# Performance work log

Measured on AMD Instinct MI355X. Metric: run time of the kernel, lower is better.

Reference implementation:

```python
import jax, jax.numpy as jnp
import numpy as np

N = 4_194_304
NUM_ITER = 6
DAMPING = 0.95
TOL = 1e-06
EPS = 1e-12


def _translate_x(dx):
    """4x4 homogeneous translation along the optical (x) axis."""
    return jnp.eye(4, dtype=dx.dtype).at[0, 3].set(dx)


def setup_inputs() -> dict:
    key = jax.random.key(0)
    k1, k2, k3 = jax.random.split(key, 3)
    # Ray origins: near x = -10, transverse spread within/around the aperture
    px = -10.0 + 0.5 * jax.random.normal(k1, (N, 1), dtype=jnp.float32)
    pyz = 8.0 * jax.random.normal(k2, (N, 2), dtype=jnp.float32)
    P = jnp.concatenate([px, pyz], axis=-1)
    # Ray directions: mostly +x, small transverse components, normalized
    vyz = 0.05 * jax.random.normal(k3, (N, 2), dtype=jnp.float32)
    V = jnp.concatenate([jnp.ones((N, 1), jnp.float32), vyz], axis=-1)
    V = V / jnp.linalg.norm(V, axis=-1, keepdims=True)
    tf = jnp.eye(4, dtype=jnp.float32)
    return {
        "P": P,
        "V": V,
        "tf": tf,
        "diameter": jnp.float32(50.0),
        "C": jnp.float32(0.02),
        "anchors": jnp.zeros((2,), jnp.float32),
        "scale": jnp.float32(1.0),
        "normalize": jnp.asarray(False),
    }


def reference(P, V, tf, diameter, C, anchors, scale, normalize):
    # normalize: curvature interpreted relative to semi-diameter
    C_eff = jnp.where(normalize, C * 2.0 / diameter, C)
    s2 = scale * scale

    def sag(r2):  # scaled spherical sag: f = scale * g(r2/scale^2)
        u = r2 / s2
        root = jnp.sqrt(jnp.clip(1.0 - C_eff * C_eff * u, EPS))
        return scale * C_eff * u / (1.0 + root)

    def sag_grad(y, z):  # (df/dy, df/dz) = C*(y,z) / (scale*sqrt(1-C^2 u))
        u = (y * y + z * z) / s2
        root = jnp.sqrt(jnp.clip(1.0 - C_eff * C_eff * u, EPS))
        k = C_eff / (scale * root)
        return k * y, k * z

    # anchors shift the surface along x by fractions of the edge sag (extent)
    extent = sag(jnp.square(diameter * 0.5))
    surface_tf = tf @ _translate_x(-anchors[0] * extent)
    next_tf = tf @ _translate_x((anchors[1] - anchors[0]) * extent)

    # Rays into surface-local frame
    R = surface_tf[:3, :3]
    tv = surface_tf[:3, 3]
    Pl = (P - tv) @ R  # [N,3] = R^T (P - t)
    Vl = V @ R
    vx, vy, vz = Vl[:, 0], Vl[:, 1], Vl[:, 2]

    safe_vx = jnp.where(jnp.abs(vx) > EPS, vx, EPS)
    t = -Pl[:, 0] / safe_vx  # init: intersection with plane x=0

    # Damped Newton on F(t) = sag(y(t),z(t)) - x(t)
    for _ in range(NUM_ITER):
        p = Pl + t[:, None] * Vl
        y, z = p[:, 1], p[:, 2]
        F = sag(y * y + z * z) - p[:, 0]
        gy, gz = sag_grad(y, z)
        dF = gy * vy + gz * vz - vx
        dF = jnp.where(jnp.abs(dF) > EPS, dF, EPS)
        t = t - DAMPING * F / dF

    p = Pl + t[:, None] * Vl
    y, z = p[:, 1], p[:, 2]
    r2 = y * y + z * z
    F = sag(r2) - p[:, 0]
    gy, gz = sag_grad(y, z)
    # implicit-surface normal: grad(sag(y,z) - x) = (-1, gy, gz), normalized
    n_local = jnp.stack([-jnp.ones_like(gy), gy, gz], axis=-1)
    n_local = n_local / jnp.linalg.norm(n_local, axis=-1, keepdims=True)
    normals = n_local @ R.T  # back to global frame

    valid = (r2 <= jnp.square(diameter * 0.5)) & (jnp.abs(F) < 100.0 * TOL)
    return t, normals, valid, surface_tf, next_tf
```

## Files before the change

### kernel.cpp

```cpp
#include <hip/hip_runtime.h>

#define F_EPS 1e-12f
#define F_DAMPING 0.95f
#define N_ITER 6
#define TPB 256

__launch_bounds__(TPB)
__global__ void trace_kernel(const float* __restrict__ P,
                             const float* __restrict__ V,
                             const float* __restrict__ tf,
                             const float* __restrict__ diameter,
                             const float* __restrict__ Cc,
                             const float* __restrict__ anchors,
                             const float* __restrict__ scale_p,
                             const unsigned char* __restrict__ normalize,
                             float* __restrict__ out,
                             int n)
{
    __shared__ float4 sbuf[TPB * 3];
    const int tid  = threadIdx.x;
    const int base = (blockIdx.x * TPB + tid) * 4;

    float R0,R1,R2,R3,R4,R5,R6,R7,R8, tv0,tv1,tv2;
    float C_eff, scale, half_d2, inv_s2;
    {
#pragma clang fp contract(off)
        float d  = diameter[0];
        float c  = Cc[0];
        float sc = scale_p[0];
        bool  nrm = (normalize[0] != 0);
        C_eff = nrm ? (c * 2.0f / d) : c;
        float s2 = sc * sc;
        float hr = d * 0.5f;
        half_d2 = hr * hr;
        float u = half_d2 / s2;
        float root = sqrtf(fmaxf(1.0f - (C_eff * C_eff) * u, F_EPS));
        float extent = sc * C_eff * u / (1.0f + root);
        float a0 = anchors[0], a1 = anchors[1];
        float dx0 = -a0 * extent;
        float dx1 = (a1 - a0) * extent;
        R0 = tf[0]; R1 = tf[1]; R2 = tf[2];
        R3 = tf[4]; R4 = tf[5]; R5 = tf[6];
        R6 = tf[8]; R7 = tf[9]; R8 = tf[10];
        tv0 = tf[0] * dx0 + tf[3];
        tv1 = tf[4] * dx0 + tf[7];
        tv2 = tf[8] * dx0 + tf[11];
        scale  = sc;
        inv_s2 = 1.0f / s2;
        if (blockIdx.x == 0 && tid < 16) {
            int i = tid >> 2, j = tid & 3;
            float v  = tf[tid];
            float sv = (j == 3) ? (tf[i * 4] * dx0 + v) : v;
            float nv = (j == 3) ? (tf[i * 4] * dx1 + v) : v;
            float* out_tail = out + (size_t)n * 5;
            out_tail[tid]      = sv;
            out_tail[16 + tid] = nv;
        }
    }
    float ce2   = C_eff * C_eff;
    float sC    = scale * C_eff;
    float a_num = sC * inv_s2;
    float ce2s  = ce2 * inv_s2;
    float Cs    = C_eff / scale;

    const bool full_block = ((blockIdx.x + 1) * (TPB * 4) <= n);

    float Px[4], Py[4], Pz[4], Vx[4], Vy[4], Vz[4];
    if (full_block) {
        const size_t bf4 = (size_t)blockIdx.x * (TPB * 3);
        const float4* P4 = reinterpret_cast<const float4*>(P);
        const float4* V4 = reinterpret_cast<const float4*>(V);
        float4 p0 = P4[bf4 + tid], p1 = P4[bf4 + TPB + tid], p2 = P4[bf4 + 2*TPB + tid];
        float4 q0 = V4[bf4 + tid], q1 = V4[bf4 + TPB + tid], q2 = V4[bf4 + 2*TPB + tid];
        sbuf[tid] = p0; sbuf[TPB + tid] = p1; sbuf[2*TPB + tid] = p2;
        __syncthreads();
        float4 a = sbuf[3*tid], b = sbuf[3*tid + 1], c = sbuf[3*tid + 2];
        __syncthreads();
        Px[0]=a.x; Py[0]=a.y; Pz[0]=a.z; Px[1]=a.w; Py[1]=b.x; Pz[1]=b.y;
        Px[2]=b.z; Py[2]=b.w; Pz[2]=c.x; Px[3]=c.y; Py[3]=c.z; Pz[3]=c.w;
        sbuf[tid] = q0; sbuf[TPB + tid] = q1; sbuf[2*TPB + tid] = q2;
        __syncthreads();
        a = sbuf[3*tid]; b = sbuf[3*tid + 1]; c = sbuf[3*tid + 2];
        __syncthreads();
        Vx[0]=a.x; Vy[0]=a.y; Vz[0]=a.z; Vx[1]=a.w; Vy[1]=b.x; Vz[1]=b.y;
        Vx[2]=b.z; Vy[2]=b.w; Vz[2]=c.x; Vx[3]=c.y; Vy[3]=c.z; Vz[3]=c.w;
    } else {
        for (int r = 0; r < 4; ++r) {
            int i = base + r;
            if (i < n) {
                Px[r] = P[(size_t)i*3 + 0]; Py[r] = P[(size_t)i*3 + 1]; Pz[r] = P[(size_t)i*3 + 2];
                Vx[r] = V[(size_t)i*3 + 0]; Vy[r] = V[(size_t)i*3 + 1]; Vz[r] = V[(size_t)i*3 + 2];
            } else {
                Px[r] = 0.0f; Py[r] = 0.0f; Pz[r] = 0.0f;
                Vx[r] = 1.0f; Vy[r] = 0.0f; Vz[r] = 0.0f;
            }
        }
    }

    float Plx[4], Ply[4], Plz[4], vx[4], vy[4], vz[4], tN[4];
#pragma unroll
    for (int r = 0; r < 4; ++r) {
        float px0 = Px[r] - tv0, py0 = Py[r] - tv1, pz0 = Pz[r] - tv2;
        Plx[r] = px0 * R0 + py0 * R3 + pz0 * R6;
        Ply[r] = px0 * R1 + py0 * R4 + pz0 * R7;
        Plz[r] = px0 * R2 + py0 * R5 + pz0 * R8;
        vx[r] = Vx[r] * R0 + Vy[r] * R3 + Vz[r] * R6;
        vy[r] = Vx[r] * R1 + Vy[r] * R4 + Vz[r] * R7;
        vz[r] = Vx[r] * R2 + Vy[r] * R5 + Vz[r] * R8;
        float safe_vx = (fabsf(vx[r]) > F_EPS) ? vx[r] : F_EPS;
        tN[r] = (-Plx[r]) * __builtin_amdgcn_rcpf(safe_vx);
    }

#pragma unroll
    for (int it = 0; it < N_ITER; ++it) {
#pragma unroll
        for (int r = 0; r < 4; ++r) {
            float pxx = fmaf(tN[r], vx[r], Plx[r]);
            float py  = fmaf(tN[r], vy[r], Ply[r]);
            float pz  = fmaf(tN[r], vz[r], Plz[r]);
            float r2  = fmaf(py, py, pz * pz);
            float m   = fmaxf(fmaf(-ce2s, r2, 1.0f), F_EPS);
            float rsq = __builtin_amdgcn_rsqf(m);
            float root = m * rsq;
            float k    = Cs * rsq;
            float ird  = __builtin_amdgcn_rcpf(1.0f + root);
            float F    = fmaf(a_num * r2, ird, -pxx);
            float dF = fmaf(k * py, vy[r], fmaf(k * pz, vz[r], -vx[r]));
            dF = (fabsf(dF) > F_EPS) ? dF : F_EPS;
            tN[r] = fmaf(-F_DAMPING * F, __builtin_amdgcn_rcpf(dF), tN[r]);
        }
    }

    float tres[4], nxo[4], nyo[4], nzo[4], val[4];
#pragma unroll
    for (int r = 0; r < 4; ++r) {
        float pxx = fmaf(tN[r], vx[r], Plx[r]);
        float py  = fmaf(tN[r], vy[r], Ply[r]);
        float pz  = fmaf(tN[r], vz[r], Plz[r]);
        float r2  = fmaf(py, py, pz * pz);
        float m   = fmaxf(fmaf(-ce2s, r2, 1.0f), F_EPS);
        float rsq = __builtin_amdgcn_rsqf(m);
        float root = m * rsq;
        float k    = Cs * rsq;
        float ird  = __builtin_amdgcn_rcpf(1.0f + root);
        float F    = fmaf(a_num * r2, ird, -pxx);
        float gy = k * py, gz = k * pz;
        float nn2 = fmaf(gy, gy, fmaf(gz, gz, 1.0f));
        float irn = __builtin_amdgcn_rsqf(nn2);
        float nlx = -irn, nly = gy * irn, nlz = gz * irn;
        nxo[r] = nlx * R0 + nly * R1 + nlz * R2;
        nyo[r] = nlx * R3 + nly * R4 + nlz * R5;
        nzo[r] = nlx * R6 + nly * R7 + nlz * R8;
        tres[r] = tN[r];
        val[r]  = ((r2 <= half_d2) && (fabsf(F) < 1e-4f)) ? 1.0f : 0.0f;
    }

    float* t_out = out;
    float* n_out = out + (size_t)n;
    float* v_out = out + (size_t)n * 4;
    if (full_block) {
        sbuf[3*tid]     = make_float4(nxo[0], nyo[0], nzo[0], nxo[1]);
        sbuf[3*tid + 1] = make_float4(nyo[1], nzo[1], nxo[2], nyo[2]);
        sbuf[3*tid + 2] = make_float4(nzo[2], nxo[3], nyo[3], nzo[3]);
        __syncthreads();
        const size_t bf4 = (size_t)blockIdx.x * (TPB * 3);
        float4* N4 = reinterpret_cast<float4*>(n_out);
        N4[bf4 + tid]         = sbuf[tid];
        N4[bf4 + TPB + tid]   = sbuf[TPB + tid];
        N4[bf4 + 2*TPB + tid] = sbuf[2*TPB + tid];
        *reinterpret_cast<float4*>(t_out + base) = make_float4(tres[0], tres[1], tres[2], tres[3]);
        *reinterpret_cast<float4*>(v_out + base) = make_float4(val[0], val[1], val[2], val[3]);
    } else {
        for (int r = 0; r < 4; ++r) {
            int i = base + r;
            if (i < n) {
                t_out[i] = tres[r];
                n_out[(size_t)i*3 + 0] = nxo[r];
                n_out[(size_t)i*3 + 1] = nyo[r];
                n_out[(size_t)i*3 + 2] = nzo[r];
                v_out[i] = val[r];
            }
        }
    }
}

extern "C" void kernel_launch(void* const* d_in, const int* in_sizes, int n_in,
                              void* d_out, int out_size, void* d_ws, size_t ws_size,
                              hipStream_t stream) {
    const float* P  = (const float*)d_in[0];
    const float* V  = (const float*)d_in[1];
    const float* tf = (const float*)d_in[2];
    const float* diameter = (const float*)d_in[3];
    const float* C  = (const float*)d_in[4];
    const float* anchors = (const float*)d_in[5];
    const float* scale = (const float*)d_in[6];
    const unsigned char* normalize = (const unsigned char*)d_in[7];
    int n = in_sizes[0] / 3;
    float* out = (float*)d_out;

    int rays_per_block = TPB * 4;
    int blocks = (n + rays_per_block - 1) / rays_per_block;
    trace_kernel<<<blocks, TPB, 0, stream>>>(P, V, tf, diameter, C, anchors, scale,
                                             normalize, out, n);
}
```

Measured before the change: 177.1 us.

## Process four tiles per block with register prefetch, drop LDS transpose

Each block now handles four tiles of rays and prefetches the next tile's P/V into registers while computing the current one, giving a software-pipelined loop. The shared-memory transpose and its barriers are removed: each thread loads its own three contiguous float4s directly and writes normals the same way. This cuts the grid size by four and hides load latency behind compute. The cost is higher register pressure and per-thread strided float4 accesses that coalesce less well than the old LDS-staged pattern.

```diff
diff --git a/kernel.cpp b/kernel.cpp
--- a/kernel.cpp
+++ b/kernel.cpp
@@ -4,6 +4,7 @@
 #define F_DAMPING 0.95f
 #define N_ITER 6
 #define TPB 256
+#define TILES 4
 
 __launch_bounds__(TPB)
 __global__ void trace_kernel(const float* __restrict__ P,
@@ -17,9 +18,7 @@
                              float* __restrict__ out,
                              int n)
 {
-    __shared__ float4 sbuf[TPB * 3];
-    const int tid  = threadIdx.x;
-    const int base = (blockIdx.x * TPB + tid) * 4;
+    const int tid = threadIdx.x;
 
     float R0,R1,R2,R3,R4,R5,R6,R7,R8, tv0,tv1,tv2;
     float C_eff, scale, half_d2, inv_s2;
@@ -57,130 +56,167 @@
             out_tail[16 + tid] = nv;
         }
     }
-    float ce2   = C_eff * C_eff;
-    float sC    = scale * C_eff;
-    float a_num = sC * inv_s2;
-    float ce2s  = ce2 * inv_s2;
-    float Cs    = C_eff / scale;
-
-    const bool full_block = ((blockIdx.x + 1) * (TPB * 4) <= n);
-
-    float Px[4], Py[4], Pz[4], Vx[4], Vy[4], Vz[4];
-    if (full_block) {
-        const size_t bf4 = (size_t)blockIdx.x * (TPB * 3);
-        const float4* P4 = reinterpret_cast<const float4*>(P);
-        const float4* V4 = reinterpret_cast<const float4*>(V);
-        float4 p0 = P4[bf4 + tid], p1 = P4[bf4 + TPB + tid], p2 = P4[bf4 + 2*TPB + tid];
-        float4 q0 = V4[bf4 + tid], q1 = V4[bf4 + TPB + tid], q2 = V4[bf4 + 2*TPB + tid];
-        sbuf[tid] = p0; sbuf[TPB + tid] = p1; sbuf[2*TPB + tid] = p2;
-        __syncthreads();
-        float4 a = sbuf[3*tid], b = sbuf[3*tid + 1], c = sbuf[3*tid + 2];
-        __syncthreads();
-        Px[0]=a.x; Py[0]=a.y; Pz[0]=a.z; Px[1]=a.w; Py[1]=b.x; Pz[1]=b.y;
-        Px[2]=b.z; Py[2]=b.w; Pz[2]=c.x; Px[3]=c.y; Py[3]=c.z; Pz[3]=c.w;
-        sbuf[tid] = q0; sbuf[TPB + tid] = q1; sbuf[2*TPB + tid] = q2;
-        __syncthreads();
-        a = sbuf[3*tid]; b = sbuf[3*tid + 1]; c = sbuf[3*tid + 2];
-        __syncthreads();
-        Vx[0]=a.x; Vy[0]=a.y; Vz[0]=a.z; Vx[1]=a.w; Vy[1]=b.x; Vz[1]=b.y;
-        Vx[2]=b.z; Vy[2]=b.w; Vz[2]=c.x; Vx[3]=c.y; Vy[3]=c.z; Vz[3]=c.w;
-    } else {
-        for (int r = 0; r < 4; ++r) {
-            int i = base + r;
-            if (i < n) {
-                Px[r] = P[(size_t)i*3 + 0]; Py[r] = P[(size_t)i*3 + 1]; Pz[r] = P[(size_t)i*3 + 2];
-                Vx[r] = V[(size_t)i*3 + 0]; Vy[r] = V[(size_t)i*3 + 1]; Vz[r] = V[(size_t)i*3 + 2];
-            } else {
-                Px[r] = 0.0f; Py[r] = 0.0f; Pz[r] = 0.0f;
-                Vx[r] = 1.0f; Vy[r] = 0.0f; Vz[r] = 0.0f;
-            }
-        }
-    }
-
-    float Plx[4], Ply[4], Plz[4], vx[4], vy[4], vz[4], tN[4];
-#pragma unroll
-    for (int r = 0; r < 4; ++r) {
-        float px0 = Px[r] - tv0, py0 = Py[r] - tv1, pz0 = Pz[r] - tv2;
-        Plx[r] = px0 * R0 + py0 * R3 + pz0 * R6;
-        Ply[r] = px0 * R1 + py0 * R4 + pz0 * R7;
-        Plz[r] = px0 * R2 + py0 * R5 + pz0 * R8;
-        vx[r] = Vx[r] * R0 + Vy[r] * R3 + Vz[r] * R6;
-        vy[r] = Vx[r] * R1 + Vy[r] * R4 + Vz[r] * R7;
-        vz[r] = Vx[r] * R2 + Vy[r] * R5 + Vz[r] * R8;
-        float safe_vx = (fabsf(vx[r]) > F_EPS) ? vx[r] : F_EPS;
-        tN[r] = (-Plx[r]) * __builtin_amdgcn_rcpf(safe_vx);
-    }
-
-#pragma unroll
-    for (int it = 0; it < N_ITER; ++it) {
-#pragma unroll
-        for (int r = 0; r < 4; ++r) {
-            float pxx = fmaf(tN[r], vx[r], Plx[r]);
-            float py  = fmaf(tN[r], vy[r], Ply[r]);
-            float pz  = fmaf(tN[r], vz[r], Plz[r]);
-            float r2  = fmaf(py, py, pz * pz);
-            float m   = fmaxf(fmaf(-ce2s, r2, 1.0f), F_EPS);
-            float rsq = __builtin_amdgcn_rsqf(m);
-            float root = m * rsq;
-            float k    = Cs * rsq;
-            float ird  = __builtin_amdgcn_rcpf(1.0f + root);
-            float F    = fmaf(a_num * r2, ird, -pxx);
-            float dF = fmaf(k * py, vy[r], fmaf(k * pz, vz[r], -vx[r]));
-            dF = (fabsf(dF) > F_EPS) ? dF : F_EPS;
-            tN[r] = fmaf(-F_DAMPING * F, __builtin_amdgcn_rcpf(dF), tN[r]);
-        }
-    }
-
-    float tres[4], nxo[4], nyo[4], nzo[4], val[4];
-#pragma unroll
-    for (int r = 0; r < 4; ++r) {
-        float pxx = fmaf(tN[r], vx[r], Plx[r]);
-        float py  = fmaf(tN[r], vy[r], Ply[r]);
-        float pz  = fmaf(tN[r], vz[r], Plz[r]);
-        float r2  = fmaf(py, py, pz * pz);
-        float m   = fmaxf(fmaf(-ce2s, r2, 1.0f), F_EPS);
-        float rsq = __builtin_amdgcn_rsqf(m);
-        float root = m * rsq;
-        float k    = Cs * rsq;
-        float ird  = __builtin_amdgcn_rcpf(1.0f + root);
-        float F    = fmaf(a_num * r2, ird, -pxx);
-        float gy = k * py, gz = k * pz;
-        float nn2 = fmaf(gy, gy, fmaf(gz, gz, 1.0f));
-        float irn = __builtin_amdgcn_rsqf(nn2);
-        float nlx = -irn, nly = gy * irn, nlz = gz * irn;
-        nxo[r] = nlx * R0 + nly * R1 + nlz * R2;
-        nyo[r] = nlx * R3 + nly * R4 + nlz * R5;
-        nzo[r] = nlx * R6 + nly * R7 + nlz * R8;
-        tres[r] = tN[r];
-        val[r]  = ((r2 <= half_d2) && (fabsf(F) < 1e-4f)) ? 1.0f : 0.0f;
-    }
-
+    const float ce2   = C_eff * C_eff;
+    const float sC    = scale * C_eff;
+    const float a_num = sC * inv_s2;
+    const float ce2s  = ce2 * inv_s2;
+    const float Cs    = C_eff / scale;
+
+    const float4* P4 = reinterpret_cast<const float4*>(P);
+    const float4* V4 = reinterpret_cast<const float4*>(V);
     float* t_out = out;
     float* n_out = out + (size_t)n;
     float* v_out = out + (size_t)n * 4;
-    if (full_block) {
-        sbuf[3*tid]     = make_float4(nxo[0], nyo[0], nzo[0], nxo[1]);
-        sbuf[3*tid + 1] = make_float4(nyo[1], nzo[1], nxo[2], nyo[2]);
-        sbuf[3*tid + 2] = make_float4(nzo[2], nxo[3], nyo[3], nzo[3]);
-        __syncthreads();
-        const size_t bf4 = (size_t)blockIdx.x * (TPB * 3);
-        float4* N4 = reinterpret_cast<float4*>(n_out);
-        N4[bf4 + tid]         = sbuf[tid];
-        N4[bf4 + TPB + tid]   = sbuf[TPB + tid];
-        N4[bf4 + 2*TPB + tid] = sbuf[2*TPB + tid];
-        *reinterpret_cast<float4*>(t_out + base) = make_float4(tres[0], tres[1], tres[2], tres[3]);
-        *reinterpret_cast<float4*>(v_out + base) = make_float4(val[0], val[1], val[2], val[3]);
-    } else {
-        for (int r = 0; r < 4; ++r) {
-            int i = base + r;
-            if (i < n) {
-                t_out[i] = tres[r];
-                n_out[(size_t)i*3 + 0] = nxo[r];
-                n_out[(size_t)i*3 + 1] = nyo[r];
-                n_out[(size_t)i*3 + 2] = nzo[r];
-                v_out[i] = val[r];
-            }
-        }
+
+
+    float4 c0,c1,c2,c3,c4,c5;
+    float4 x0,x1,x2,x3,x4,x5;
+
+    {
+        size_t u = ((size_t)blockIdx.x * TILES + 0) * TPB + tid;
+        long base = (long)u * 4;
+        if (base + 4 <= n) {
+            c0 = P4[u*3+0]; c1 = P4[u*3+1]; c2 = P4[u*3+2];
+            c3 = V4[u*3+0]; c4 = V4[u*3+1]; c5 = V4[u*3+2];
+        } else {
+            float tmp[12];
+            for (int r = 0; r < 4; ++r) {
+                long i = base + r;
+                if (i < n) {
+                    tmp[r*3+0] = P[i*3+0]; tmp[r*3+1] = P[i*3+1]; tmp[r*3+2] = P[i*3+2];
+                } else { tmp[r*3+0] = 0.0f; tmp[r*3+1] = 0.0f; tmp[r*3+2] = 0.0f; }
+            }
+            c0 = make_float4(tmp[0],tmp[1],tmp[2],tmp[3]);
+            c1 = make_float4(tmp[4],tmp[5],tmp[6],tmp[7]);
+            c2 = make_float4(tmp[8],tmp[9],tmp[10],tmp[11]);
+            for (int r = 0; r < 4; ++r) {
+                long i = base + r;
+                if (i < n) {
+                    tmp[r*3+0] = V[i*3+0]; tmp[r*3+1] = V[i*3+1]; tmp[r*3+2] = V[i*3+2];
+                } else { tmp[r*3+0] = 1.0f; tmp[r*3+1] = 0.0f; tmp[r*3+2] = 0.0f; }
+            }
+            c3 = make_float4(tmp[0],tmp[1],tmp[2],tmp[3]);
+            c4 = make_float4(tmp[4],tmp[5],tmp[6],tmp[7]);
+            c5 = make_float4(tmp[8],tmp[9],tmp[10],tmp[11]);
+        }
+    }
+
+#pragma unroll
+    for (int j = 0; j < TILES; ++j) {
+        if (j + 1 < TILES) {
+            size_t u1 = ((size_t)blockIdx.x * TILES + (j+1)) * TPB + tid;
+            long base1 = (long)u1 * 4;
+            if (base1 + 4 <= n) {
+                x0 = P4[u1*3+0]; x1 = P4[u1*3+1]; x2 = P4[u1*3+2];
+                x3 = V4[u1*3+0]; x4 = V4[u1*3+1]; x5 = V4[u1*3+2];
+            } else {
+                x0 = make_float4(0,0,0,0); x1 = x0; x2 = x0;
+                x3 = make_float4(1,0,0,1); x4 = make_float4(0,0,1,0); x5 = make_float4(0,0,1,0);
+                for (int r = 0; r < 4; ++r) {
+                    long i = base1 + r;
+                    if (i < n) {
+                        float px = P[i*3+0], py = P[i*3+1], pz = P[i*3+2];
+                        float qx = V[i*3+0], qy = V[i*3+1], qz = V[i*3+2];
+                        if (r==0) { x0.x=px; x0.y=py; x0.z=pz; x3.x=qx; x3.y=qy; x3.z=qz; }
+                        if (r==1) { x0.w=px; x1.x=py; x1.y=pz; x3.w=qx; x4.x=qy; x4.y=qz; }
+                        if (r==2) { x1.z=px; x1.w=py; x2.x=pz; x4.z=qx; x4.w=qy; x5.x=qz; }
+                        if (r==3) { x2.y=px; x2.z=py; x2.w=pz; x5.y=qx; x5.z=qy; x5.w=qz; }
+                    }
+                }
+            }
+        }
+
+        size_t u = ((size_t)blockIdx.x * TILES + j) * TPB + tid;
+        long base = (long)u * 4;
+        if (base < n) {
+            float Px[4], Py[4], Pz[4], Vx[4], Vy[4], Vz[4];
+            Px[0]=c0.x; Py[0]=c0.y; Pz[0]=c0.z; Px[1]=c0.w; Py[1]=c1.x; Pz[1]=c1.y;
+            Px[2]=c1.z; Py[2]=c1.w; Pz[2]=c2.x; Px[3]=c2.y; Py[3]=c2.z; Pz[3]=c2.w;
+            Vx[0]=c3.x; Vy[0]=c3.y; Vz[0]=c3.z; Vx[1]=c3.w; Vy[1]=c4.x; Vz[1]=c4.y;
+            Vx[2]=c4.z; Vy[2]=c4.w; Vz[2]=c5.x; Vx[3]=c5.y; Vy[3]=c5.z; Vz[3]=c5.w;
+            if (base + 4 > n) {
+                for (int r = 0; r < 4; ++r)
+                    if (base + r >= n) { Px[r]=0; Py[r]=0; Pz[r]=0; Vx[r]=1; Vy[r]=0; Vz[r]=0; }
+            }
+
+            float Plx[4], Ply[4], Plz[4], vx[4], vy[4], vz[4], tN[4];
+#pragma unroll
+            for (int r = 0; r < 4; ++r) {
+                float px0 = Px[r] - tv0, py0 = Py[r] - tv1, pz0 = Pz[r] - tv2;
+                Plx[r] = px0 * R0 + py0 * R3 + pz0 * R6;
+                Ply[r] = px0 * R1 + py0 * R4 + pz0 * R7;
+                Plz[r] = px0 * R2 + py0 * R5 + pz0 * R8;
+                vx[r] = Vx[r] * R0 + Vy[r] * R3 + Vz[r] * R6;
+                vy[r] = Vx[r] * R1 + Vy[r] * R4 + Vz[r] * R7;
+                vz[r] = Vx[r] * R2 + Vy[r] * R5 + Vz[r] * R8;
+                float safe_vx = (fabsf(vx[r]) > F_EPS) ? vx[r] : F_EPS;
+                tN[r] = (-Plx[r]) * __builtin_amdgcn_rcpf(safe_vx);
+            }
+#pragma unroll
+            for (int it = 0; it < N_ITER; ++it) {
+#pragma unroll
+                for (int r = 0; r < 4; ++r) {
+                    float pxx = fmaf(tN[r], vx[r], Plx[r]);
+                    float py  = fmaf(tN[r], vy[r], Ply[r]);
+                    float pz  = fmaf(tN[r], vz[r], Plz[r]);
+                    float r2  = fmaf(py, py, pz * pz);
+                    float m   = fmaxf(fmaf(-ce2s, r2, 1.0f), F_EPS);
+                    float rsq = __builtin_amdgcn_rsqf(m);
+                    float root = m * rsq;
+                    float k    = Cs * rsq;
+                    float ird  = __builtin_amdgcn_rcpf(1.0f + root);
+                    float F    = fmaf(a_num * r2, ird, -pxx);
+                    float dF = fmaf(k * py, vy[r], fmaf(k * pz, vz[r], -vx[r]));
+                    dF = (fabsf(dF) > F_EPS) ? dF : F_EPS;
+                    tN[r] = fmaf(-F_DAMPING * F, __builtin_amdgcn_rcpf(dF), tN[r]);
+                }
+            }
+            float tres[4], nxo[4], nyo[4], nzo[4], val[4];
+#pragma unroll
+            for (int r = 0; r < 4; ++r) {
+                float pxx = fmaf(tN[r], vx[r], Plx[r]);
+                float py  = fmaf(tN[r], vy[r], Ply[r]);
+                float pz  = fmaf(tN[r], vz[r], Plz[r]);
+                float r2  = fmaf(py, py, pz * pz);
+                float m   = fmaxf(fmaf(-ce2s, r2, 1.0f), F_EPS);
+                float rsq = __builtin_amdgcn_rsqf(m);
+                float root = m * rsq;
+                float k    = Cs * rsq;
+                float ird  = __builtin_amdgcn_rcpf(1.0f + root);
+                float F    = fmaf(a_num * r2, ird, -pxx);
+                float gy = k * py, gz = k * pz;
+                float nn2 = fmaf(gy, gy, fmaf(gz, gz, 1.0f));
+                float irn = __builtin_amdgcn_rsqf(nn2);
+                float nlx = -irn, nly = gy * irn, nlz = gz * irn;
+                nxo[r] = nlx * R0 + nly * R1 + nlz * R2;
+                nyo[r] = nlx * R3 + nly * R4 + nlz * R5;
+                nzo[r] = nlx * R6 + nly * R7 + nlz * R8;
+                tres[r] = tN[r];
+                val[r]  = ((r2 <= half_d2) && (fabsf(F) < 1e-4f)) ? 1.0f : 0.0f;
+            }
+
+            if (base + 4 <= n) {
+                reinterpret_cast<float4*>(t_out)[u] = make_float4(tres[0], tres[1], tres[2], tres[3]);
+                float4* N4 = reinterpret_cast<float4*>(n_out);
+                N4[u*3+0] = make_float4(nxo[0], nyo[0], nzo[0], nxo[1]);
+                N4[u*3+1] = make_float4(nyo[1], nzo[1], nxo[2], nyo[2]);
+                N4[u*3+2] = make_float4(nzo[2], nxo[3], nyo[3], nzo[3]);
+                reinterpret_cast<float4*>(v_out)[u] = make_float4(val[0], val[1], val[2], val[3]);
+            } else {
+                for (int r = 0; r < 4; ++r) {
+                    long i = base + r;
+                    if (i < n) {
+                        t_out[i] = tres[r];
+                        n_out[i*3+0] = nxo[r];
+                        n_out[i*3+1] = nyo[r];
+                        n_out[i*3+2] = nzo[r];
+                        v_out[i] = val[r];
+                    }
+                }
+            }
+        }
+
+        c0 = x0; c1 = x1; c2 = x2; c3 = x3; c4 = x4; c5 = x5;
     }
 }
 
@@ -198,8 +234,8 @@
     int n = in_sizes[0] / 3;
     float* out = (float*)d_out;
 
-    int rays_per_block = TPB * 4;
-    int blocks = (n + rays_per_block - 1) / rays_per_block;
+    long rays_per_block = (long)TPB * 4 * TILES;
+    int blocks = (int)((n + rays_per_block - 1) / rays_per_block);
     trace_kernel<<<blocks, TPB, 0, stream>>>(P, V, tf, diameter, C, anchors, scale,
                                              normalize, out, n);
 }
```

New measurement: 185.6 us. +4.8%, slower.
